# Performance work log

Measured on AMD Instinct MI355X. Metric: run time of the kernel, lower is better.

## Reference

```python
import jax, jax.numpy as jnp
import numpy as np

DPH, NH = 64, 4           # dim_per_head, num_head -> dim_total = 256
ALPHA_CONV = 0.1          # LeakyReLU alpha in DarknetConv2D_BN_Leaky
ALPHA_DENSE = 0.3         # Keras LeakyReLU default alpha (Dense activation)


def _leaky(x, a):
    return jnp.where(x > 0, x, a * x)


def _cbl(x, W, g, b):
    """1x1 conv (no bias) + inference BatchNorm (folded affine) + LeakyReLU(0.1)."""
    y = jnp.einsum('nwhc,cd->nwhd', x, W)
    return _leaky(y * g + b, ALPHA_CONV)


def setup_inputs() -> dict:
    key = jax.random.key(0)
    ks = jax.random.split(key, 26)
    N, Wg, Hg, C = 16, 64, 64, 256
    D = DPH * NH

    def n(k, shape, s=1.0):
        return jax.random.normal(k, shape, jnp.float32) * s

    return {
        'inputs': n(ks[0], (N, Wg, Hg, C)),
        'style':  n(ks[1], (N, C)),
        'W_dense': n(ks[2], (C, C), 0.05),
        'Wq_c': n(ks[3], (C, D), 0.05), 'gq_c': 1.0 + n(ks[4], (D,), 0.02), 'bq_c': n(ks[5], (D,), 0.02),
        'Wk_c': n(ks[6], (C, D), 0.05), 'gk_c': 1.0 + n(ks[7], (D,), 0.02), 'bk_c': n(ks[8], (D,), 0.02),
        'Wv_c': n(ks[9], (C, D), 0.05), 'gv_c': 1.0 + n(ks[10], (D,), 0.02), 'bv_c': n(ks[11], (D,), 0.02),
        'Wq_p': n(ks[12], (C, D), 0.05), 'gq_p': 1.0 + n(ks[13], (D,), 0.02), 'bq_p': n(ks[14], (D,), 0.02),
        'Wk_p': n(ks[15], (C, D), 0.05), 'gk_p': 1.0 + n(ks[16], (D,), 0.02), 'bk_p': n(ks[17], (D,), 0.02),
        'Wv_p': n(ks[18], (C, D), 0.05), 'gv_p': 1.0 + n(ks[19], (D,), 0.02), 'bv_p': n(ks[20], (D,), 0.02),
        'W_ch':  n(ks[21], (2 * D, D), 0.02),
        'W_pos': n(ks[22], (2 * D, NH), 0.02),
        'W_out': n(ks[23], (2 * D, C), 0.05),
        'g_out': 1.0 + n(ks[24], (C,), 0.02),
        'b_out': n(ks[25], (C,), 0.02),
    }


def reference(inputs, style, W_dense,
              Wq_c, gq_c, bq_c, Wk_c, gk_c, bk_c, Wv_c, gv_c, bv_c,
              Wq_p, gq_p, bq_p, Wk_p, gk_p, bk_p, Wv_p, gv_p, bv_p,
              W_ch, W_pos, W_out, g_out, b_out):
    N, Wg, Hg, C = inputs.shape
    D = DPH * NH
    scale = 1.0 / jnp.sqrt(jnp.float32(DPH))

    # style -> query feature, [N,1,1,C]
    q0 = _leaky(style @ W_dense, ALPHA_DENSE)[:, None, None, :]

    # ---------- channel-wise attention branch ----------
    qc = _cbl(q0, Wq_c, gq_c, bq_c)          # [N,1,1,D]
    kc = _cbl(inputs, Wk_c, gk_c, bk_c)      # [N,W,H,D]
    vc = _cbl(inputs, Wv_c, gv_c, bv_c)      # [N,W,H,D]
    catc = jnp.concatenate([jnp.broadcast_to(qc, kc.shape), kc], axis=-1)  # [N,W,H,2D]
    # einsum('awhd,awhdc->ac') with w broadcast over a,w,h == plain contraction
    a_c = jnp.einsum('nwhd,dc->nc', catc, W_ch) * scale                     # [N,D]
    a_c = jax.nn.softmax(a_c.reshape(N, DPH, NH), axis=1).reshape(N, 1, 1, D)
    o_ch = a_c * vc                                                          # [N,W,H,D]

    # ---------- position-wise attention branch ----------
    qp = _cbl(q0, Wq_p, gq_p, bq_p)
    kp = _cbl(inputs, Wk_p, gk_p, bk_p)
    vp = _cbl(inputs, Wv_p, gv_p, bv_p)
    catp = jnp.concatenate([jnp.broadcast_to(qp, kp.shape), kp], axis=-1)   # [N,W,H,2D]
    a_p = jnp.einsum('nwhd,dm->nwhm', catp, W_pos) * scale                  # [N,W,H,NH]
    a_p = jax.nn.softmax(a_p.reshape(N, Wg * Hg, NH), axis=1)
    a_p = a_p.reshape(N, Wg, Hg, NH, 1)
    o_pos = (a_p * vp.reshape(N, Wg, Hg, NH, DPH)).reshape(N, Wg, Hg, D)

    # ---------- fuse + output 1x1 conv ----------
    out = _cbl(jnp.concatenate([o_ch, o_pos], axis=-1), W_out, g_out, b_out)  # [N,W,H,C]
    return out
```

## Files before the change

kernel.cpp:

```cpp
#include <hip/hip_runtime.h>
#include <hip/hip_bf16.h>

#define NB    16
#define NPIX  4096
#define PTOT  65536
#define SCALE 0.125f

typedef __attribute__((ext_vector_type(8))) short short8;
typedef __attribute__((ext_vector_type(4))) float f32x4;

__device__ __forceinline__ float leaky(float x, float a) { return x > 0.f ? x : a * x; }

__device__ __forceinline__ unsigned short f2bfbits(float f) {
    __hip_bfloat16 h = __float2bfloat16(f); unsigned short u;
    __builtin_memcpy(&u, &h, 2); return u;
}

__device__ __forceinline__ void gld16(const void* g, void* l) {
    __builtin_amdgcn_global_load_lds(
        (const __attribute__((address_space(1))) unsigned int*)g,
        (__attribute__((address_space(3))) unsigned int*)l, 16, 0, 0);
}

__device__ __forceinline__ void mfma_step64(const char* Aseg, const char* Bs,
                                            int l, int wm, int wn, f32x4 acc[2][4])
{
#pragma unroll
    for (int ks = 0; ks < 2; ++ks) {
        short8 af[2], bfr[4];
        const int c = ks * 4 + (l >> 4);
        const int sw = ((c ^ (l & 7)) << 4);
#pragma unroll
        for (int mf = 0; mf < 2; ++mf)
            af[mf] = *(const short8*)(Aseg + (wm * 32 + mf * 16 + (l & 15)) * 128 + sw);
#pragma unroll
        for (int nf = 0; nf < 4; ++nf)
            bfr[nf] = *(const short8*)(Bs + (wn * 64 + nf * 16 + (l & 15)) * 128 + sw);
#pragma unroll
        for (int mf = 0; mf < 2; ++mf)
#pragma unroll
            for (int nf = 0; nf < 4; ++nf)
                acc[mf][nf] = __builtin_amdgcn_mfma_f32_16x16x32_bf16(af[mf], bfr[nf], acc[mf][nf], 0, 0, 0);
    }
}

__device__ __forceinline__ void stageB(const __hip_bfloat16* Bt, int ldk, int k0,
                                       char* Bs, int w, int l, int cg)
{
#pragma unroll
    for (int pass = 0; pass < 4; ++pass) {
        const int col = w * 8 + (l >> 3) + pass * 64;
        gld16(Bt + (size_t)col * ldk + k0 + cg * 8, Bs + (w * 8 + pass * 64) * 128);
    }
}

__device__ __forceinline__ void stageA64(const __hip_bfloat16* Abf, int pix0, int k0,
                                         char* dst, int w, int l, int cg)
{
    const int row = w * 8 + (l >> 3);
    gld16(Abf + (size_t)(pix0 + row) * 256 + k0 + cg * 8, dst + w * 8 * 128);
}

template<int MODE>
__device__ __forceinline__ void k1_body(int bb, int t,
    const float* __restrict__ vin, const float* __restrict__ W,
    const float* __restrict__ g, const float* __restrict__ bv,
    float* __restrict__ vout, float* s0, float (*pr)[32])
{
    const int n = bb >> 3, c0 = (bb & 7) * 32;
    if (t < 256) s0[t] = vin[n * 256 + t];
    __syncthreads();
    const int kp = t >> 5, ci = t & 31, c = c0 + ci;
    float a = 0.f;
#pragma unroll 8
    for (int i = 0; i < 32; ++i) {
        const int k = kp * 32 + i;
        a += s0[k] * W[k * 256 + c];
    }
    pr[kp][ci] = a;
    __syncthreads();
    if (t < 32) {
        float s = 0.f;
#pragma unroll
        for (int q = 0; q < 8; ++q) s += pr[q][t];
        const int cc = c0 + t;
        if constexpr (MODE == 0)      vout[n * 256 + cc] = leaky(s, 0.3f);
        else if constexpr (MODE == 1) vout[n * 256 + cc] = leaky(s * g[cc] + bv[cc], 0.1f);
        else                          vout[n * 256 + cc] = 4096.f * s;
    }
}

template<int MODE>
__global__ __launch_bounds__(256) void k1g(
    const float* __restrict__ vin, const float* __restrict__ W,
    const float* __restrict__ g, const float* __restrict__ bv,
    float* __restrict__ vout)
{
    __shared__ float s0[256];
    __shared__ float pr[8][32];
    k1_body<MODE>(blockIdx.x, threadIdx.x, vin, W, g, bv, vout, s0, pr);
}

__global__ __launch_bounds__(256) void kIW_cvt(
    const float* __restrict__ in, __hip_bfloat16* __restrict__ out,
    const float* __restrict__ W0, const float* __restrict__ W1,
    const float* __restrict__ W2, const float* __restrict__ W3,
    const float* __restrict__ Wout,
    __hip_bfloat16* __restrict__ WT4, __hip_bfloat16* __restrict__ WoutT,
    const float* __restrict__ style, const float* __restrict__ W_dense,
    float* __restrict__ s1ws)
{
    __shared__ float s0[256];
    __shared__ float pr[8][32];
    const int b = blockIdx.x, t = threadIdx.x;
    if (b < 2048) {
        const size_t stride = (size_t)2048 * 256 * 8;
        for (size_t i0 = ((size_t)b * 256 + t) * 8; i0 < (size_t)PTOT * 256; i0 += stride) {
            const float4 a = *(const float4*)(in + i0);
            const float4 c = *(const float4*)(in + i0 + 4);
            short8 v;
            v[0]=(short)f2bfbits(a.x); v[1]=(short)f2bfbits(a.y); v[2]=(short)f2bfbits(a.z); v[3]=(short)f2bfbits(a.w);
            v[4]=(short)f2bfbits(c.x); v[5]=(short)f2bfbits(c.y); v[6]=(short)f2bfbits(c.z); v[7]=(short)f2bfbits(c.w);
            *(short8*)(out + i0) = v;
        }
    } else if (b < 3072) {
        const int bb = b - 2048;
        const int w = bb >> 8, c = bb & 255;
        const float* W = (w == 0) ? W0 : (w == 1) ? W1 : (w == 2) ? W2 : W3;
        WT4[((size_t)w * 256 + c) * 256 + t] = __float2bfloat16(W[t * 256 + c]);
    } else if (b < 3328) {
        const int c = b - 3072;
        WoutT[(size_t)c * 512 + t]       = __float2bfloat16(Wout[t * 256 + c]);
        WoutT[(size_t)c * 512 + t + 256] = __float2bfloat16(Wout[(t + 256) * 256 + c]);
    } else {
        k1_body<0>(b - 3328, t, style, W_dense, nullptr, nullptr, s1ws, s0, pr);
    }
}

__global__ __launch_bounds__(512, 4) void kA(
    const __hip_bfloat16* __restrict__ Abf,
    const __hip_bfloat16* __restrict__ BkcT, const __hip_bfloat16* __restrict__ BkpT,
    const float* __restrict__ gkc, const float* __restrict__ bkc,
    const float* __restrict__ gkp, const float* __restrict__ bkp,
    const float* __restrict__ W_pos,
    float* __restrict__ partial, float* __restrict__ logits)
{
    __shared__ alignas(16) char smem[73728];
    char* Afull = smem;
    char* Bs    = smem + 32768;
    float* wpos_s = (float*)(smem + 65536);
    float* red    = (float*)(smem + 69632);
    float* sc     = (float*)(smem + 69632);

    const int t = threadIdx.x, l = t & 63, w = t >> 6;
    const int wm = w >> 2, wn = w & 3;
    const int pix0 = blockIdx.x * 64;
    const int cg = (l & 7) ^ ((l >> 3) & 7);

    for (int e = t; e < 1024; e += 512) wpos_s[e] = W_pos[1024 + e];

#pragma unroll
    for (int s = 0; s < 4; ++s)
        stageA64(Abf, pix0, s * 64, Afull + s * 8192, w, l, cg);

    f32x4 acc[2][4];
#pragma unroll
    for (int i = 0; i < 2; ++i)
#pragma unroll
        for (int j = 0; j < 4; ++j) acc[i][j] = (f32x4)0.f;
    for (int s = 0; s < 4; ++s) {
        __syncthreads();
        stageB(BkcT, 256, s * 64, Bs, w, l, cg);
        __syncthreads();
        mfma_step64(Afull + s * 8192, Bs, l, wm, wn, acc);
    }
#pragma unroll
    for (int nf = 0; nf < 4; ++nf) {
        const int col = wn * 64 + nf * 16 + (l & 15);
        const float g = gkc[col], bb = bkc[col];
        float cs = 0.f;
#pragma unroll
        for (int mf = 0; mf < 2; ++mf)
#pragma unroll
            for (int r = 0; r < 4; ++r) cs += leaky(acc[mf][nf][r] * g + bb, 0.1f);
        cs += __shfl_xor(cs, 16);
        cs += __shfl_xor(cs, 32);
        if (l < 16) red[wm * 256 + wn * 64 + nf * 16 + l] = cs;
    }
    __syncthreads();
    if (t < 256) partial[(size_t)blockIdx.x * 256 + t] = red[t] + red[256 + t];

#pragma unroll
    for (int i = 0; i < 2; ++i)
#pragma unroll
        for (int j = 0; j < 4; ++j) acc[i][j] = (f32x4)0.f;
    for (int s = 0; s < 4; ++s) {
        __syncthreads();
        stageB(BkpT, 256, s * 64, Bs, w, l, cg);
        __syncthreads();
        mfma_step64(Afull + s * 8192, Bs, l, wm, wn, acc);
    }
    __syncthreads();
#pragma unroll
    for (int mf = 0; mf < 2; ++mf)
#pragma unroll
        for (int r = 0; r < 4; ++r) {
            const int row_l = wm * 32 + mf * 16 + (l >> 4) * 4 + r;
            float pm0 = 0.f, pm1 = 0.f, pm2 = 0.f, pm3 = 0.f;
#pragma unroll
            for (int nf = 0; nf < 4; ++nf) {
                const int col = wn * 64 + nf * 16 + (l & 15);
                const float g = gkp[col], bb = bkp[col];
                const float v = leaky(acc[mf][nf][r] * g + bb, 0.1f);
                pm0 += v * wpos_s[col * 4 + 0];
                pm1 += v * wpos_s[col * 4 + 1];
                pm2 += v * wpos_s[col * 4 + 2];
                pm3 += v * wpos_s[col * 4 + 3];
            }
#pragma unroll
            for (int mask = 1; mask <= 8; mask <<= 1) {
                pm0 += __shfl_xor(pm0, mask);
                pm1 += __shfl_xor(pm1, mask);
                pm2 += __shfl_xor(pm2, mask);
                pm3 += __shfl_xor(pm3, mask);
            }
            if ((l & 15) == 0) {
                float* sp = &sc[row_l * 16 + wn];
                sp[0] = pm0; sp[4] = pm1; sp[8] = pm2; sp[12] = pm3;
            }
        }
    __syncthreads();
    if (t < 256) {
        const int row = t >> 2, m = t & 3;
        const float sum = sc[row * 16 + m * 4 + 0] + sc[row * 16 + m * 4 + 1]
                        + sc[row * 16 + m * 4 + 2] + sc[row * 16 + m * 4 + 3];
        logits[(size_t)(pix0 + row) * 4 + m] = SCALE * sum;
    }
}

__global__ __launch_bounds__(256) void k2bc(
    const float* __restrict__ partial,
    const float* __restrict__ acq, const float* __restrict__ W_ch,
    float* __restrict__ a_c, float* __restrict__ lg)
{
    const int t = threadIdx.x;
    if (blockIdx.x < 16) {
        __shared__ float ks[256], lgs[256];
        const int n = blockIdx.x;
        float s = 0.f;
        for (int tt = 0; tt < 64; ++tt) s += partial[(size_t)(n * 64 + tt) * 256 + t];
        ks[t] = s;
        __syncthreads();
        float bot = 0.f;
        for (int d = 0; d < 256; ++d) bot += ks[d] * W_ch[(256 + d) * 256 + t];
        const float L = SCALE * (acq[n * 256 + t] + bot);
        lgs[t] = L;
        __syncthreads();
        const int nh = t & 3;
        float mx = -1e30f;
        for (int i = 0; i < 64; ++i) mx = fmaxf(mx, lgs[i * 4 + nh]);
        float sum = 0.f;
        for (int i = 0; i < 64; ++i) sum += __expf(lgs[i * 4 + nh] - mx);
        a_c[n * 256 + t] = __expf(L - mx) / sum;
    } else {
        __shared__ float r[256];
        const int bb = blockIdx.x - 16;
        const int n = bb >> 2, m = bb & 3;
        const int base = n * 4096;
        float v[16];
        float mx = -1e30f;
#pragma unroll
        for (int i = 0; i < 16; ++i) {
            v[i] = lg[(size_t)(base + i * 256 + t) * 4 + m];
            mx = fmaxf(mx, v[i]);
        }
        r[t] = mx; __syncthreads();
        for (int s = 128; s > 0; s >>= 1) { if (t < s) r[t] = fmaxf(r[t], r[t + s]); __syncthreads(); }
        mx = r[0]; __syncthreads();
        float sum = 0.f;
#pragma unroll
        for (int i = 0; i < 16; ++i) { v[i] = __expf(v[i] - mx); sum += v[i]; }
        r[t] = sum; __syncthreads();
        for (int s = 128; s > 0; s >>= 1) { if (t < s) r[t] += r[t + s]; __syncthreads(); }
        const float rinv = 1.f / r[0];
#pragma unroll
        for (int i = 0; i < 16; ++i) lg[(size_t)(base + i * 256 + t) * 4 + m] = v[i] * rinv;
    }
}

__global__ __launch_bounds__(512, 4) void kB(
    const __hip_bfloat16* __restrict__ Abf,
    const __hip_bfloat16* __restrict__ BvcT, const __hip_bfloat16* __restrict__ BvpT,
    const __hip_bfloat16* __restrict__ WoutT,
    const float* __restrict__ gvc, const float* __restrict__ bvc,
    const float* __restrict__ gvp, const float* __restrict__ bvp,
    const float* __restrict__ a_c, const float* __restrict__ apos,
    const float* __restrict__ g_out, const float* __restrict__ b_out,
    float* __restrict__ outp)
{
    __shared__ alignas(16) char smem[75776];
    char* As   = smem;
    char* Bs   = smem + 8192;
    char* A2   = smem + 40960;
    float* ac_s = (float*)(smem + 73728);
    float* ap_s = (float*)(smem + 74752);

    const int t = threadIdx.x, l = t & 63, w = t >> 6;
    const int wm = w >> 2, wn = w & 3;
    const int pix0 = blockIdx.x * 64;
    const int n = pix0 >> 12;
    const int cg = (l & 7) ^ ((l >> 3) & 7);

    if (t < 256) {
        ac_s[t] = a_c[n * 256 + t];
        ap_s[t] = apos[(size_t)pix0 * 4 + t];
    }

    f32x4 acc2[2][4];
#pragma unroll
    for (int i = 0; i < 2; ++i)
#pragma unroll
        for (int j = 0; j < 4; ++j) acc2[i][j] = (f32x4)0.f;

    for (int half = 0; half < 2; ++half) {
        const __hip_bfloat16* Bv = half ? BvpT : BvcT;
        const float* gv = half ? gvp : gvc;
        const float* bv = half ? bvp : bvc;

        f32x4 acc1[2][4];
#pragma unroll
        for (int i = 0; i < 2; ++i)
#pragma unroll
            for (int j = 0; j < 4; ++j) acc1[i][j] = (f32x4)0.f;
        for (int s = 0; s < 4; ++s) {
            __syncthreads();
            stageA64(Abf, pix0, s * 64, As, w, l, cg);
            stageB(Bv, 256, s * 64, Bs, w, l, cg);
            __syncthreads();
            mfma_step64(As, Bs, l, wm, wn, acc1);
        }
        __syncthreads();
#pragma unroll
        for (int nf = 0; nf < 4; ++nf) {
            const int col = wn * 64 + nf * 16 + (l & 15);
            const float g = gv[col], bb = bv[col];
            const int c2 = (col & 63) >> 3, cb = (col & 7) * 2;
            const float sc_c = ac_s[col];
#pragma unroll
            for (int mf = 0; mf < 2; ++mf)
#pragma unroll
                for (int r = 0; r < 4; ++r) {
                    const int row = wm * 32 + mf * 16 + (l >> 4) * 4 + r;
                    float v = leaky(acc1[mf][nf][r] * g + bb, 0.1f);
                    v *= half ? ap_s[row * 4 + wn] : sc_c;
                    *(unsigned short*)(A2 + wn * 8192 + row * 128
                                       + ((c2 ^ (row & 7)) << 4) + cb) = f2bfbits(v);
                }
        }
        for (int s = 0; s < 4; ++s) {
            __syncthreads();
            stageB(WoutT, 512, half * 256 + s * 64, Bs, w, l, cg);
            __syncthreads();
            mfma_step64(A2 + s * 8192, Bs, l, wm, wn, acc2);
        }
    }

#pragma unroll
    for (int nf = 0; nf < 4; ++nf) {
        const int col = wn * 64 + nf * 16 + (l & 15);
        const float g = g_out[col], bb = b_out[col];
#pragma unroll
        for (int mf = 0; mf < 2; ++mf)
#pragma unroll
            for (int r = 0; r < 4; ++r) {
                const int p = pix0 + wm * 32 + mf * 16 + (l >> 4) * 4 + r;
                outp[(size_t)p * 256 + col] = leaky(acc2[mf][nf][r] * g + bb, 0.1f);
            }
    }
}

extern "C" void kernel_launch(void* const* d_in, const int* in_sizes, int n_in,
                              void* d_out, int out_size, void* d_ws, size_t ws_size,
                              hipStream_t stream)
{
    const float* inputs  = (const float*)d_in[0];
    const float* style   = (const float*)d_in[1];
    const float* W_dense = (const float*)d_in[2];
    const float* Wq_c = (const float*)d_in[3];
    const float* gq_c = (const float*)d_in[4];
    const float* bq_c = (const float*)d_in[5];
    const float* Wk_c = (const float*)d_in[6];
    const float* gk_c = (const float*)d_in[7];
    const float* bk_c = (const float*)d_in[8];
    const float* Wv_c = (const float*)d_in[9];
    const float* gv_c = (const float*)d_in[10];
    const float* bv_c = (const float*)d_in[11];
    const float* Wk_p = (const float*)d_in[15];
    const float* gk_p = (const float*)d_in[16];
    const float* bk_p = (const float*)d_in[17];
    const float* Wv_p = (const float*)d_in[18];
    const float* gv_p = (const float*)d_in[19];
    const float* bv_p = (const float*)d_in[20];
    const float* W_ch  = (const float*)d_in[21];
    const float* W_pos = (const float*)d_in[22];
    const float* W_out = (const float*)d_in[23];
    const float* g_out = (const float*)d_in[24];
    const float* b_out = (const float*)d_in[25];

    float* ws = (float*)d_ws;
    float* s1ws    = ws;
    float* qcws    = ws + 4096;
    float* acq     = ws + 8192;
    float* a_c     = ws + 12288;
    float* partial = ws + 16384;
    float* logits  = ws + 278528;
    __hip_bfloat16* in_bf = (__hip_bfloat16*)(ws + 540672);
    __hip_bfloat16* WT4   = (__hip_bfloat16*)(ws + 8929280);
    __hip_bfloat16* WoutT = (__hip_bfloat16*)(ws + 9060352);

    kIW_cvt<<<3456, 256, 0, stream>>>(inputs, in_bf, Wk_c, Wv_c, Wk_p, Wv_p, W_out,
                                      WT4, WoutT, style, W_dense, s1ws);
    k1g<1><<<128, 256, 0, stream>>>(s1ws, Wq_c, gq_c, bq_c, qcws);
    k1g<2><<<128, 256, 0, stream>>>(qcws, W_ch, nullptr, nullptr, acq);

    kA<<<1024, 512, 0, stream>>>(in_bf, WT4, WT4 + 2 * 65536,
                                 gk_c, bk_c, gk_p, bk_p, W_pos, partial, logits);

    k2bc<<<80, 256, 0, stream>>>(partial, acq, W_ch, a_c, logits);

    kB<<<1024, 512, 0, stream>>>(in_bf, WT4 + 65536, WT4 + 3 * 65536, WoutT,
                                 gv_c, bv_c, gv_p, bv_p, a_c, logits,
                                 g_out, b_out, (float*)d_out);
}
```

Measured before the change: 146.6 us.

## Fuse input bf16 conversion into GEMM kernels and double-buffer K-slices

Removes the separate full-tensor fp32-to-bf16 conversion pass, so kA and kB read fp32 inputs directly and convert while staging into LDS. This drops one write and one read of a 32 MB bf16 copy of the input. The K loops switch from 64-wide single-buffered steps with two barriers each to 32-wide double-buffered steps with one barrier, so the next slice loads while the MFMAs run on the current one. kA and kB now each read the fp32 input (twice the bytes of the bf16 copy), and kB's A loads go through registers and only 256 of the 512 threads.

After: 152.7 us. 1.04x slower.

```diff
diff --git a/kernel.cpp b/kernel.cpp
--- a/kernel.cpp
+++ b/kernel.cpp
@@ -1,8 +1,6 @@
 #include <hip/hip_runtime.h>
 #include <hip/hip_bf16.h>
 
-#define NB    16
-#define NPIX  4096
 #define PTOT  65536
 #define SCALE 0.125f
 
@@ -22,43 +20,79 @@
         (__attribute__((address_space(3))) unsigned int*)l, 16, 0, 0);
 }
 
-__device__ __forceinline__ void mfma_step64(const char* Aseg, const char* Bs,
+
+__device__ __forceinline__ void stageB32(const __hip_bfloat16* Bt, int ldk, int k0,
+                                         char* BsBuf, int w, int l)
+{
+    const int cg = (l & 3) ^ ((l >> 3) & 3);
+#pragma unroll
+    for (int p = 0; p < 2; ++p) {
+        const int col = w * 16 + p * 128 + (l >> 2);
+        gld16(Bt + (size_t)col * ldk + k0 + cg * 8, BsBuf + (w * 16 + p * 128) * 64);
+    }
+}
+
+__device__ __forceinline__ void loadA32(const float* in, int pix0, int k0, int t,
+                                        float4& a0, float4& a1)
+{
+    const int row = t >> 2, c = t & 3;
+    const float* p = in + (size_t)(pix0 + row) * 256 + k0 + c * 8;
+    a0 = *(const float4*)p;
+    a1 = *(const float4*)(p + 4);
+}
+__device__ __forceinline__ void writeA32(char* AsBuf, int t, const float4& a0, const float4& a1)
+{
+    const int row = t >> 2, c = t & 3;
+    short8 v;
+    v[0]=(short)f2bfbits(a0.x); v[1]=(short)f2bfbits(a0.y); v[2]=(short)f2bfbits(a0.z); v[3]=(short)f2bfbits(a0.w);
+    v[4]=(short)f2bfbits(a1.x); v[5]=(short)f2bfbits(a1.y); v[6]=(short)f2bfbits(a1.z); v[7]=(short)f2bfbits(a1.w);
+    *(short8*)(AsBuf + row * 64 + ((c ^ ((row >> 1) & 3)) << 4)) = v;
+}
+
+__device__ __forceinline__ void mfma32_AB64(const char* AsBuf, const char* BsBuf,
                                             int l, int wm, int wn, f32x4 acc[2][4])
 {
-#pragma unroll
-    for (int ks = 0; ks < 2; ++ks) {
-        short8 af[2], bfr[4];
-        const int c = ks * 4 + (l >> 4);
-        const int sw = ((c ^ (l & 7)) << 4);
-#pragma unroll
-        for (int mf = 0; mf < 2; ++mf)
-            af[mf] = *(const short8*)(Aseg + (wm * 32 + mf * 16 + (l & 15)) * 128 + sw);
+    const int c = l >> 4;
+    short8 af[2], bfr[4];
+#pragma unroll
+    for (int mf = 0; mf < 2; ++mf) {
+        const int row = wm * 32 + mf * 16 + (l & 15);
+        af[mf] = *(const short8*)(AsBuf + row * 64 + ((c ^ ((row >> 1) & 3)) << 4));
+    }
+#pragma unroll
+    for (int nf = 0; nf < 4; ++nf) {
+        const int row = wn * 64 + nf * 16 + (l & 15);
+        bfr[nf] = *(const short8*)(BsBuf + row * 64 + ((c ^ ((row >> 1) & 3)) << 4));
+    }
+#pragma unroll
+    for (int mf = 0; mf < 2; ++mf)
 #pragma unroll
         for (int nf = 0; nf < 4; ++nf)
-            bfr[nf] = *(const short8*)(Bs + (wn * 64 + nf * 16 + (l & 15)) * 128 + sw);
-#pragma unroll
-        for (int mf = 0; mf < 2; ++mf)
-#pragma unroll
-            for (int nf = 0; nf < 4; ++nf)
-                acc[mf][nf] = __builtin_amdgcn_mfma_f32_16x16x32_bf16(af[mf], bfr[nf], acc[mf][nf], 0, 0, 0);
-    }
-}
-
-__device__ __forceinline__ void stageB(const __hip_bfloat16* Bt, int ldk, int k0,
-                                       char* Bs, int w, int l, int cg)
-{
-#pragma unroll
-    for (int pass = 0; pass < 4; ++pass) {
-        const int col = w * 8 + (l >> 3) + pass * 64;
-        gld16(Bt + (size_t)col * ldk + k0 + cg * 8, Bs + (w * 8 + pass * 64) * 128);
-    }
-}
-
-__device__ __forceinline__ void stageA64(const __hip_bfloat16* Abf, int pix0, int k0,
-                                         char* dst, int w, int l, int cg)
-{
-    const int row = w * 8 + (l >> 3);
-    gld16(Abf + (size_t)(pix0 + row) * 256 + k0 + cg * 8, dst + w * 8 * 128);
+            acc[mf][nf] = __builtin_amdgcn_mfma_f32_16x16x32_bf16(af[mf], bfr[nf], acc[mf][nf], 0, 0, 0);
+}
+
+__device__ __forceinline__ void mfma32_A128(const char* A128, int s, const char* BsBuf,
+                                            int l, int wm, int wn, f32x4 acc[2][4])
+{
+    const int c8 = (s & 1) * 4 + (l >> 4);
+    const int cb = l >> 4;
+    const char* Aseg = A128 + (s >> 1) * 8192;
+    short8 af[2], bfr[4];
+#pragma unroll
+    for (int mf = 0; mf < 2; ++mf) {
+        const int row = wm * 32 + mf * 16 + (l & 15);
+        af[mf] = *(const short8*)(Aseg + row * 128 + ((c8 ^ (row & 7)) << 4));
+    }
+#pragma unroll
+    for (int nf = 0; nf < 4; ++nf) {
+        const int row = wn * 64 + nf * 16 + (l & 15);
+        bfr[nf] = *(const short8*)(BsBuf + row * 64 + ((cb ^ ((row >> 1) & 3)) << 4));
+    }
+#pragma unroll
+    for (int mf = 0; mf < 2; ++mf)
+#pragma unroll
+        for (int nf = 0; nf < 4; ++nf)
+            acc[mf][nf] = __builtin_amdgcn_mfma_f32_16x16x32_bf16(af[mf], bfr[nf], acc[mf][nf], 0, 0, 0);
 }
 
 template<int MODE>
@@ -101,8 +135,7 @@
     k1_body<MODE>(blockIdx.x, threadIdx.x, vin, W, g, bv, vout, s0, pr);
 }
 
-__global__ __launch_bounds__(256) void kIW_cvt(
-    const float* __restrict__ in, __hip_bfloat16* __restrict__ out,
+__global__ __launch_bounds__(256) void kW_cvt(
     const float* __restrict__ W0, const float* __restrict__ W1,
     const float* __restrict__ W2, const float* __restrict__ W3,
     const float* __restrict__ Wout,
@@ -113,39 +146,28 @@
     __shared__ float s0[256];
     __shared__ float pr[8][32];
     const int b = blockIdx.x, t = threadIdx.x;
-    if (b < 2048) {
-        const size_t stride = (size_t)2048 * 256 * 8;
-        for (size_t i0 = ((size_t)b * 256 + t) * 8; i0 < (size_t)PTOT * 256; i0 += stride) {
-            const float4 a = *(const float4*)(in + i0);
-            const float4 c = *(const float4*)(in + i0 + 4);
-            short8 v;
-            v[0]=(short)f2bfbits(a.x); v[1]=(short)f2bfbits(a.y); v[2]=(short)f2bfbits(a.z); v[3]=(short)f2bfbits(a.w);
-            v[4]=(short)f2bfbits(c.x); v[5]=(short)f2bfbits(c.y); v[6]=(short)f2bfbits(c.z); v[7]=(short)f2bfbits(c.w);
-            *(short8*)(out + i0) = v;
-        }
-    } else if (b < 3072) {
-        const int bb = b - 2048;
-        const int w = bb >> 8, c = bb & 255;
+    if (b < 1024) {
+        const int w = b >> 8, c = b & 255;
         const float* W = (w == 0) ? W0 : (w == 1) ? W1 : (w == 2) ? W2 : W3;
         WT4[((size_t)w * 256 + c) * 256 + t] = __float2bfloat16(W[t * 256 + c]);
-    } else if (b < 3328) {
-        const int c = b - 3072;
+    } else if (b < 1280) {
+        const int c = b - 1024;
         WoutT[(size_t)c * 512 + t]       = __float2bfloat16(Wout[t * 256 + c]);
         WoutT[(size_t)c * 512 + t + 256] = __float2bfloat16(Wout[(t + 256) * 256 + c]);
     } else {
-        k1_body<0>(b - 3328, t, style, W_dense, nullptr, nullptr, s1ws, s0, pr);
+        k1_body<0>(b - 1280, t, style, W_dense, nullptr, nullptr, s1ws, s0, pr);
     }
 }
 
 __global__ __launch_bounds__(512, 4) void kA(
-    const __hip_bfloat16* __restrict__ Abf,
+    const float* __restrict__ in,
     const __hip_bfloat16* __restrict__ BkcT, const __hip_bfloat16* __restrict__ BkpT,
     const float* __restrict__ gkc, const float* __restrict__ bkc,
     const float* __restrict__ gkp, const float* __restrict__ bkp,
     const float* __restrict__ W_pos,
     float* __restrict__ partial, float* __restrict__ logits)
 {
-    __shared__ alignas(16) char smem[73728];
+    __shared__ alignas(16) char smem[71680];
     char* Afull = smem;
     char* Bs    = smem + 32768;
     float* wpos_s = (float*)(smem + 65536);
@@ -155,25 +177,38 @@
     const int t = threadIdx.x, l = t & 63, w = t >> 6;
     const int wm = w >> 2, wn = w & 3;
     const int pix0 = blockIdx.x * 64;
-    const int cg = (l & 7) ^ ((l >> 3) & 7);
 
     for (int e = t; e < 1024; e += 512) wpos_s[e] = W_pos[1024 + e];
 
-#pragma unroll
-    for (int s = 0; s < 4; ++s)
-        stageA64(Abf, pix0, s * 64, Afull + s * 8192, w, l, cg);
+    {
+        const int row = t >> 3, c = t & 7;
+#pragma unroll
+        for (int seg = 0; seg < 4; ++seg) {
+            const float* p = in + (size_t)(pix0 + row) * 256 + seg * 64 + c * 8;
+            const float4 x0 = *(const float4*)p, x1 = *(const float4*)(p + 4);
+            short8 v;
+            v[0]=(short)f2bfbits(x0.x); v[1]=(short)f2bfbits(x0.y); v[2]=(short)f2bfbits(x0.z); v[3]=(short)f2bfbits(x0.w);
+            v[4]=(short)f2bfbits(x1.x); v[5]=(short)f2bfbits(x1.y); v[6]=(short)f2bfbits(x1.z); v[7]=(short)f2bfbits(x1.w);
+            *(short8*)(Afull + seg * 8192 + row * 128 + ((c ^ (row & 7)) << 4)) = v;
+        }
+    }
 
     f32x4 acc[2][4];
 #pragma unroll
     for (int i = 0; i < 2; ++i)
 #pragma unroll
         for (int j = 0; j < 4; ++j) acc[i][j] = (f32x4)0.f;
-    for (int s = 0; s < 4; ++s) {
-        __syncthreads();
-        stageB(BkcT, 256, s * 64, Bs, w, l, cg);
-        __syncthreads();
-        mfma_step64(Afull + s * 8192, Bs, l, wm, wn, acc);
-    }
+
+    stageB32(BkcT, 256, 0, Bs, w, l);
+    __syncthreads();
+    int cur = 0;
+    for (int s = 0; s < 8; ++s) {
+        if (s < 7) stageB32(BkcT, 256, (s + 1) * 32, Bs + (cur ^ 1) * 16384, w, l);
+        mfma32_A128(Afull, s, Bs + cur * 16384, l, wm, wn, acc);
+        __syncthreads();
+        cur ^= 1;
+    }
+    stageB32(BkpT, 256, 0, Bs, w, l);
 #pragma unroll
     for (int nf = 0; nf < 4; ++nf) {
         const int col = wn * 64 + nf * 16 + (l & 15);
@@ -194,13 +229,13 @@
     for (int i = 0; i < 2; ++i)
 #pragma unroll
         for (int j = 0; j < 4; ++j) acc[i][j] = (f32x4)0.f;
-    for (int s = 0; s < 4; ++s) {
-        __syncthreads();
-        stageB(BkpT, 256, s * 64, Bs, w, l, cg);
-        __syncthreads();
-        mfma_step64(Afull + s * 8192, Bs, l, wm, wn, acc);
-    }
-    __syncthreads();
+    cur = 0;
+    for (int s = 0; s < 8; ++s) {
+        if (s < 7) stageB32(BkpT, 256, (s + 1) * 32, Bs + (cur ^ 1) * 16384, w, l);
+        mfma32_A128(Afull, s, Bs + cur * 16384, l, wm, wn, acc);
+        __syncthreads();
+        cur ^= 1;
+    }
 #pragma unroll
     for (int mf = 0; mf < 2; ++mf)
 #pragma unroll
@@ -289,7 +324,7 @@
 }
 
 __global__ __launch_bounds__(512, 4) void kB(
-    const __hip_bfloat16* __restrict__ Abf,
+    const float* __restrict__ in,
     const __hip_bfloat16* __restrict__ BvcT, const __hip_bfloat16* __restrict__ BvpT,
     const __hip_bfloat16* __restrict__ WoutT,
     const float* __restrict__ gvc, const float* __restrict__ bvc,
@@ -309,7 +344,6 @@
     const int wm = w >> 2, wn = w & 3;
     const int pix0 = blockIdx.x * 64;
     const int n = pix0 >> 12;
-    const int cg = (l & 7) ^ ((l >> 3) & 7);
 
     if (t < 256) {
         ac_s[t] = a_c[n * 256 + t];
@@ -332,14 +366,28 @@
         for (int i = 0; i < 2; ++i)
 #pragma unroll
             for (int j = 0; j < 4; ++j) acc1[i][j] = (f32x4)0.f;
-        for (int s = 0; s < 4; ++s) {
+
+        if (t < 256) {
+            float4 a0, a1;
+            loadA32(in, pix0, 0, t, a0, a1);
+            writeA32(As, t, a0, a1);
+        }
+        stageB32(Bv, 256, 0, Bs, w, l);
+        __syncthreads();
+        int cur = 0;
+        for (int s = 0; s < 8; ++s) {
+            float4 a0, a1;
+            const bool st = (s < 7);
+            if (st) {
+                if (t < 256) loadA32(in, pix0, (s + 1) * 32, t, a0, a1);
+                stageB32(Bv, 256, (s + 1) * 32, Bs + (cur ^ 1) * 16384, w, l);
+            }
+            mfma32_AB64(As + cur * 4096, Bs + cur * 16384, l, wm, wn, acc1);
+            if (st && t < 256) writeA32(As + (cur ^ 1) * 4096, t, a0, a1);
             __syncthreads();
-            stageA64(Abf, pix0, s * 64, As, w, l, cg);
-            stageB(Bv, 256, s * 64, Bs, w, l, cg);
-            __syncthreads();
-            mfma_step64(As, Bs, l, wm, wn, acc1);
-        }
-        __syncthreads();
+            cur ^= 1;
+        }
+
 #pragma unroll
         for (int nf = 0; nf < 4; ++nf) {
             const int col = wn * 64 + nf * 16 + (l & 15);
@@ -357,11 +405,14 @@
                                        + ((c2 ^ (row & 7)) << 4) + cb) = f2bfbits(v);
                 }
         }
-        for (int s = 0; s < 4; ++s) {
+        stageB32(WoutT, 512, half * 256, Bs, w, l);
+        __syncthreads();
+        int curg = 0;
+        for (int s = 0; s < 8; ++s) {
+            if (s < 7) stageB32(WoutT, 512, half * 256 + (s + 1) * 32, Bs + (curg ^ 1) * 16384, w, l);
+            mfma32_A128(A2, s, Bs + curg * 16384, l, wm, wn, acc2);
             __syncthreads();
-            stageB(WoutT, 512, half * 256 + s * 64, Bs, w, l, cg);
-            __syncthreads();
-            mfma_step64(A2 + s * 8192, Bs, l, wm, wn, acc2);
+            curg ^= 1;
         }
     }
 
@@ -414,21 +465,20 @@
     float* a_c     = ws + 12288;
     float* partial = ws + 16384;
     float* logits  = ws + 278528;
-    __hip_bfloat16* in_bf = (__hip_bfloat16*)(ws + 540672);
-    __hip_bfloat16* WT4   = (__hip_bfloat16*)(ws + 8929280);
-    __hip_bfloat16* WoutT = (__hip_bfloat16*)(ws + 9060352);
-
-    kIW_cvt<<<3456, 256, 0, stream>>>(inputs, in_bf, Wk_c, Wv_c, Wk_p, Wv_p, W_out,
-                                      WT4, WoutT, style, W_dense, s1ws);
+    __hip_bfloat16* WT4   = (__hip_bfloat16*)(ws + 540672);
+    __hip_bfloat16* WoutT = (__hip_bfloat16*)(ws + 671744);
+
+    kW_cvt<<<1408, 256, 0, stream>>>(Wk_c, Wv_c, Wk_p, Wv_p, W_out,
+                                     WT4, WoutT, style, W_dense, s1ws);
     k1g<1><<<128, 256, 0, stream>>>(s1ws, Wq_c, gq_c, bq_c, qcws);
     k1g<2><<<128, 256, 0, stream>>>(qcws, W_ch, nullptr, nullptr, acq);
 
-    kA<<<1024, 512, 0, stream>>>(in_bf, WT4, WT4 + 2 * 65536,
+    kA<<<1024, 512, 0, stream>>>(inputs, WT4, WT4 + 2 * 65536,
                                  gk_c, bk_c, gk_p, bk_p, W_pos, partial, logits);
 
     k2bc<<<80, 256, 0, stream>>>(partial, acq, W_ch, a_c, logits);
 
-    kB<<<1024, 512, 0, stream>>>(in_bf, WT4 + 65536, WT4 + 3 * 65536, WoutT,
+    kB<<<1024, 512, 0, stream>>>(inputs, WT4 + 65536, WT4 + 3 * 65536, WoutT,
                                  gv_c, bv_c, gv_p, bv_p, a_c, logits,
                                  g_out, b_out, (float*)d_out);
 }
```

## Fuse input bf16 conversion into kA and stage output through LDS for coalesced stores

Applied to the files above, without the earlier changes.

The separate pass that converted the full fp32 input to bf16 is removed. kA now reads fp32 input directly, converts it in registers, writes it into its swizzled LDS tile, and also writes the bf16 copy to global memory for later use by kB. Separately, kB's epilogue now stages the output tile in shared memory and writes it with 16-byte vector stores, replacing the scattered scalar stores. The first change drops one full read of the input tensor and one kernel launch. The cost is that kA does synchronous fp32 loads in place of async LDS loads, and kB gains extra barriers.

New measurement: 147.0 us. About the same (+0.3%).

```diff
diff --git a/kernel.cpp b/kernel.cpp
--- a/kernel.cpp
+++ b/kernel.cpp
@@ -1,8 +1,6 @@
 #include <hip/hip_runtime.h>
 #include <hip/hip_bf16.h>
 
-#define NB    16
-#define NPIX  4096
 #define PTOT  65536
 #define SCALE 0.125f
 
@@ -101,8 +99,7 @@
     k1_body<MODE>(blockIdx.x, threadIdx.x, vin, W, g, bv, vout, s0, pr);
 }
 
-__global__ __launch_bounds__(256) void kIW_cvt(
-    const float* __restrict__ in, __hip_bfloat16* __restrict__ out,
+__global__ __launch_bounds__(256) void kW_cvt(
     const float* __restrict__ W0, const float* __restrict__ W1,
     const float* __restrict__ W2, const float* __restrict__ W3,
     const float* __restrict__ Wout,
@@ -113,32 +110,21 @@
     __shared__ float s0[256];
     __shared__ float pr[8][32];
     const int b = blockIdx.x, t = threadIdx.x;
-    if (b < 2048) {
-        const size_t stride = (size_t)2048 * 256 * 8;
-        for (size_t i0 = ((size_t)b * 256 + t) * 8; i0 < (size_t)PTOT * 256; i0 += stride) {
-            const float4 a = *(const float4*)(in + i0);
-            const float4 c = *(const float4*)(in + i0 + 4);
-            short8 v;
-            v[0]=(short)f2bfbits(a.x); v[1]=(short)f2bfbits(a.y); v[2]=(short)f2bfbits(a.z); v[3]=(short)f2bfbits(a.w);
-            v[4]=(short)f2bfbits(c.x); v[5]=(short)f2bfbits(c.y); v[6]=(short)f2bfbits(c.z); v[7]=(short)f2bfbits(c.w);
-            *(short8*)(out + i0) = v;
-        }
-    } else if (b < 3072) {
-        const int bb = b - 2048;
-        const int w = bb >> 8, c = bb & 255;
+    if (b < 1024) {
+        const int w = b >> 8, c = b & 255;
         const float* W = (w == 0) ? W0 : (w == 1) ? W1 : (w == 2) ? W2 : W3;
         WT4[((size_t)w * 256 + c) * 256 + t] = __float2bfloat16(W[t * 256 + c]);
-    } else if (b < 3328) {
-        const int c = b - 3072;
+    } else if (b < 1280) {
+        const int c = b - 1024;
         WoutT[(size_t)c * 512 + t]       = __float2bfloat16(Wout[t * 256 + c]);
         WoutT[(size_t)c * 512 + t + 256] = __float2bfloat16(Wout[(t + 256) * 256 + c]);
     } else {
-        k1_body<0>(b - 3328, t, style, W_dense, nullptr, nullptr, s1ws, s0, pr);
+        k1_body<0>(b - 1280, t, style, W_dense, nullptr, nullptr, s1ws, s0, pr);
     }
 }
 
 __global__ __launch_bounds__(512, 4) void kA(
-    const __hip_bfloat16* __restrict__ Abf,
+    const float* __restrict__ in, __hip_bfloat16* __restrict__ in_bf,
     const __hip_bfloat16* __restrict__ BkcT, const __hip_bfloat16* __restrict__ BkpT,
     const float* __restrict__ gkc, const float* __restrict__ bkc,
     const float* __restrict__ gkp, const float* __restrict__ bkp,
@@ -159,9 +145,19 @@
 
     for (int e = t; e < 1024; e += 512) wpos_s[e] = W_pos[1024 + e];
 
-#pragma unroll
-    for (int s = 0; s < 4; ++s)
-        stageA64(Abf, pix0, s * 64, Afull + s * 8192, w, l, cg);
+    {
+        const int row = t >> 3, c = t & 7;
+#pragma unroll
+        for (int seg = 0; seg < 4; ++seg) {
+            const float* p = in + (size_t)(pix0 + row) * 256 + seg * 64 + c * 8;
+            const float4 x0 = *(const float4*)p, x1 = *(const float4*)(p + 4);
+            short8 v;
+            v[0]=(short)f2bfbits(x0.x); v[1]=(short)f2bfbits(x0.y); v[2]=(short)f2bfbits(x0.z); v[3]=(short)f2bfbits(x0.w);
+            v[4]=(short)f2bfbits(x1.x); v[5]=(short)f2bfbits(x1.y); v[6]=(short)f2bfbits(x1.z); v[7]=(short)f2bfbits(x1.w);
+            *(short8*)(Afull + seg * 8192 + row * 128 + ((c ^ (row & 7)) << 4)) = v;
+            *(short8*)(in_bf + (size_t)(pix0 + row) * 256 + seg * 64 + c * 8) = v;
+        }
+    }
 
     f32x4 acc[2][4];
 #pragma unroll
@@ -365,17 +361,33 @@
         }
     }
 
+    __syncthreads();
+    float* ob = (float*)(smem + 8192);
 #pragma unroll
     for (int nf = 0; nf < 4; ++nf) {
         const int col = wn * 64 + nf * 16 + (l & 15);
         const float g = g_out[col], bb = b_out[col];
+        const int fb = col >> 2, cl = col & 3;
 #pragma unroll
         for (int mf = 0; mf < 2; ++mf)
 #pragma unroll
             for (int r = 0; r < 4; ++r) {
-                const int p = pix0 + wm * 32 + mf * 16 + (l >> 4) * 4 + r;
-                outp[(size_t)p * 256 + col] = leaky(acc2[mf][nf][r] * g + bb, 0.1f);
+                const int lrow = mf * 16 + (l >> 4) * 4 + r;
+                ob[wm * 8192 + lrow * 256 + ((fb ^ (lrow & 7)) << 2) + cl] =
+                    leaky(acc2[mf][nf][r] * g + bb, 0.1f);
             }
+    }
+    __syncthreads();
+    {
+        const int buf = t >> 8, tt = t & 255;
+        const int lrow = tt >> 3;
+        const size_t p = pix0 + buf * 32 + lrow;
+#pragma unroll
+        for (int j = 0; j < 8; ++j) {
+            const int fb = (tt & 7) + j * 8;
+            const f32x4 v4 = *(const f32x4*)&ob[buf * 8192 + lrow * 256 + ((fb ^ (lrow & 7)) << 2)];
+            *(f32x4*)(outp + p * 256 + fb * 4) = v4;
+        }
     }
 }
 
@@ -418,12 +430,12 @@
     __hip_bfloat16* WT4   = (__hip_bfloat16*)(ws + 8929280);
     __hip_bfloat16* WoutT = (__hip_bfloat16*)(ws + 9060352);
 
-    kIW_cvt<<<3456, 256, 0, stream>>>(inputs, in_bf, Wk_c, Wv_c, Wk_p, Wv_p, W_out,
-                                      WT4, WoutT, style, W_dense, s1ws);
+    kW_cvt<<<1408, 256, 0, stream>>>(Wk_c, Wv_c, Wk_p, Wv_p, W_out,
+                                     WT4, WoutT, style, W_dense, s1ws);
     k1g<1><<<128, 256, 0, stream>>>(s1ws, Wq_c, gq_c, bq_c, qcws);
     k1g<2><<<128, 256, 0, stream>>>(qcws, W_ch, nullptr, nullptr, acq);
 
-    kA<<<1024, 512, 0, stream>>>(in_bf, WT4, WT4 + 2 * 65536,
+    kA<<<1024, 512, 0, stream>>>(inputs, in_bf, WT4, WT4 + 2 * 65536,
                                  gk_c, bk_c, gk_p, bk_p, W_pos, partial, logits);
 
     k2bc<<<80, 256, 0, stream>>>(partial, acq, W_ch, a_c, logits);
```
